# Kernel optimization log

Hardware: AMD Instinct MI355X
Metric: run time of the kernel (lower is better)

## Reference

```python
import jax, jax.numpy as jnp
import numpy as np

B, S, QD, VD, H = 32, 2048, 1024, 1024, 1024
NEG = -1e9


def setup_inputs() -> dict:
    key = jax.random.key(0)
    ks = jax.random.split(key, 7)
    query = jax.random.normal(ks[0], (B, QD), dtype=jnp.float32)
    value = jax.random.normal(ks[1], (B, S, VD), dtype=jnp.float32)
    mask = jax.random.randint(ks[2], (B, S), 0, 2).astype(bool)
    # params (Linear weights stored as [in, out] for einsum convenience)
    Wq = jax.random.normal(ks[3], (QD, H), dtype=jnp.float32) / np.sqrt(QD)
    bq = jax.random.normal(ks[4], (H,), dtype=jnp.float32) * 0.01
    Wv = jax.random.normal(ks[5], (VD, H), dtype=jnp.float32) / np.sqrt(VD)
    w = jax.random.normal(ks[6], (H,), dtype=jnp.float32) / np.sqrt(H)
    return {"query": query, "value": value, "mask": mask,
            "Wq": Wq, "bq": bq, "Wv": Wv, "w": w}


def reference(query, value, mask, Wq, bq, Wv, w):
    # q-projection: [B, H]
    hq = query @ Wq + bq
    # v-projection: [B, S, H]
    hv = jnp.einsum('bsv,vh->bsh', value, Wv)
    # additive attention energies: [B, S]
    logits = jnp.einsum('bsh,h->bs', jnp.tanh(hq[:, None, :] + hv), w)
    logits = jnp.where(mask, logits, NEG)
    return jax.nn.softmax(logits, axis=-1)
```

## Files before the change

kernel.cpp:

```cpp
#include <hip/hip_runtime.h>
#include <hip/hip_bf16.h>
#include <hip/hip_fp16.h>

typedef _Float16 f16;
typedef _Float16 f16x8 __attribute__((ext_vector_type(8)));
typedef float f32x16 __attribute__((ext_vector_type(16)));
typedef unsigned int u32;

#define BB 32
#define SS 2048
#define HH 1024
#define KK 1024

#define WS_BP 0
#define WS_HQ (2u*1024u*1024u)
#define WS_LP (WS_HQ + 131072u)

__device__ __forceinline__ float tanh_f(float x) {
    float e = __expf(2.0f * x);
    return 1.0f - 2.0f * __builtin_amdgcn_rcpf(e + 1.0f);
}

__device__ __forceinline__ void gload_lds16(const void* g, void* l) {
    __builtin_amdgcn_global_load_lds(
        (const __attribute__((address_space(1))) u32*)g,
        (__attribute__((address_space(3))) u32*)l, 16, 0, 0);
}

__global__ void pack_wv(const float* __restrict__ Wv, f16* __restrict__ BP) {
    int i = blockIdx.x * 256 + threadIdx.x;
    int k = i >> 10, n = i & 1023;
    float v = Wv[i];
    int ntb = n >> 8;
    int ntl = (n >> 5) & 7;
    int kit = k >> 5;
    int ksl = (k >> 4) & 1;
    int lane = ((k >> 3) & 1) * 32 + (n & 31);
    int j = k & 7;
    BP[((((ntb * 32 + kit) * 8 + ntl) * 2 + ksl) * 64 + lane) * 8 + j] = (f16)v;
}

__global__ void hq_kernel(const float* __restrict__ query, const float* __restrict__ Wq,
                          const float* __restrict__ bq, float* __restrict__ hq) {
    int b = blockIdx.y;
    int h = (blockIdx.x & 3) * 256 + threadIdx.x;
    int v0 = (blockIdx.x >> 2) * 256;
    float acc = 0.f;
#pragma unroll 8
    for (int v = 0; v < 256; ++v)
        acc += query[b * 1024 + v0 + v] * Wq[(v0 + v) * 1024 + h];
    if (v0 == 0) acc += bq[h];
    atomicAdd(&hq[b * 1024 + h], acc);
}

__launch_bounds__(512, 4)
__global__ void fused_main(const float* __restrict__ value, const f16* __restrict__ BP,
                           const float* __restrict__ hq, const float* __restrict__ wvec,
                           float* __restrict__ lpart) {
    extern __shared__ char smem[];

    int bid = blockIdx.x;
    int tile = (bid & 7) * 256 + (bid >> 3);
    int Mt = tile >> 2, ntb = tile & 3;
    int m0 = Mt << 7;
    int b = m0 >> 11, s0 = m0 & 2047;

    int tid = threadIdx.x;
    int w = tid >> 6, l = tid & 63;
    int wm = w >> 2, wn = w & 3;
    int l31 = l & 31, lg = l >> 5;

    int arow = tid >> 2;
    const float* aga = value + (size_t)(m0 + arow) * 1024 + (tid & 3) * 8;
    int aw_off = arow * 64 + ((((tid & 3) ^ ((arow >> 1) & 3))) << 4);

    const char* bg = (const char*)BP + (size_t)ntb * (32u * 16384u) + tid * 16;

    int a_base[2], a_sw[2];
#pragma unroll
    for (int mt = 0; mt < 2; ++mt) {
        int row = wm * 64 + mt * 32 + l31;
        a_base[mt] = row * 64;
        a_sw[mt] = ((row >> 1) & 3) << 4;
    }
    int b_base[2];
#pragma unroll
    for (int nt = 0; nt < 2; ++nt)
        b_base[nt] = (wn * 2 + nt) * 2048 + l * 16;

    const f32x16 fzero = {};
    f32x16 acc[2][2];
#pragma unroll
    for (int mt = 0; mt < 2; ++mt)
#pragma unroll
        for (int nt = 0; nt < 2; ++nt) acc[mt][nt] = fzero;

    {
        const float4* ap = (const float4*)aga;
        float4 fa0 = ap[0], fa1 = ap[1];
        gload_lds16(bg, smem + 16384 + tid * 16);
        gload_lds16(bg + 8192, smem + 16384 + 8192 + tid * 16);
        union { f16 h[8]; uint4 u; } pk;
        pk.h[0] = (f16)fa0.x; pk.h[1] = (f16)fa0.y; pk.h[2] = (f16)fa0.z; pk.h[3] = (f16)fa0.w;
        pk.h[4] = (f16)fa1.x; pk.h[5] = (f16)fa1.y; pk.h[6] = (f16)fa1.z; pk.h[7] = (f16)fa1.w;
        *(uint4*)(smem + aw_off) = pk.u;
        __syncthreads();
    }

#pragma unroll 1
    for (int t = 0; t < 32; ++t) {
        const char* Acur = smem + (t & 1) * 8192;
        const char* Bcur = smem + 16384 + (t & 1) * 16384;
        char* Anx = smem + ((t + 1) & 1) * 8192;
        char* Bnx = smem + 16384 + ((t + 1) & 1) * 16384;

        float4 fa0, fa1;
        if (t < 31) {
            const float4* ap = (const float4*)(aga + (t + 1) * 32);
            fa0 = ap[0]; fa1 = ap[1];
            const char* bsrc = bg + (size_t)(t + 1) * 16384;
            gload_lds16(bsrc, Bnx + tid * 16);
            gload_lds16(bsrc + 8192, Bnx + 8192 + tid * 16);
        }

#pragma unroll
        for (int ks = 0; ks < 2; ++ks) {
            int sl = (ks * 2 + lg) << 4;
            f16x8 av0 = *(const f16x8*)(Acur + a_base[0] + (sl ^ a_sw[0]));
            f16x8 av1 = *(const f16x8*)(Acur + a_base[1] + (sl ^ a_sw[1]));
            f16x8 bv0 = *(const f16x8*)(Bcur + b_base[0] + ks * 1024);
            f16x8 bv1 = *(const f16x8*)(Bcur + b_base[1] + ks * 1024);
            acc[0][0] = __builtin_amdgcn_mfma_f32_32x32x16_f16(av0, bv0, acc[0][0], 0, 0, 0);
            acc[0][1] = __builtin_amdgcn_mfma_f32_32x32x16_f16(av0, bv1, acc[0][1], 0, 0, 0);
            acc[1][0] = __builtin_amdgcn_mfma_f32_32x32x16_f16(av1, bv0, acc[1][0], 0, 0, 0);
            acc[1][1] = __builtin_amdgcn_mfma_f32_32x32x16_f16(av1, bv1, acc[1][1], 0, 0, 0);
        }

        if (t < 31) {
            union { f16 h[8]; uint4 u; } pk;
            pk.h[0] = (f16)fa0.x; pk.h[1] = (f16)fa0.y; pk.h[2] = (f16)fa0.z; pk.h[3] = (f16)fa0.w;
            pk.h[4] = (f16)fa1.x; pk.h[5] = (f16)fa1.y; pk.h[6] = (f16)fa1.z; pk.h[7] = (f16)fa1.w;
            *(uint4*)(Anx + aw_off) = pk.u;
        }
        __syncthreads();
    }

    int h0 = ntb * 256 + wn * 64 + l31;
    int h1 = h0 + 32;
    float hq0 = hq[b * 1024 + h0], hq1 = hq[b * 1024 + h1];
    float w0 = wvec[h0], w1 = wvec[h1];

    float* part = (float*)smem;
#pragma unroll
    for (int mt = 0; mt < 2; ++mt) {
#pragma unroll
        for (int r = 0; r < 16; ++r) {
            float p = tanh_f(hq0 + acc[mt][0][r]) * w0
                    + tanh_f(hq1 + acc[mt][1][r]) * w1;
            p += __shfl_xor(p, 1); p += __shfl_xor(p, 2); p += __shfl_xor(p, 4);
            p += __shfl_xor(p, 8); p += __shfl_xor(p, 16);
            if (l31 == 0) {
                int row = wm * 64 + mt * 32 + (r & 3) + ((r >> 2) << 3) + (lg << 2);
                part[wn * 128 + row] = p;
            }
        }
    }
    __syncthreads();
    if (tid < 128) {
        float s = part[tid] + part[128 + tid] + part[256 + tid] + part[384 + tid];
        lpart[((size_t)ntb * 32 + b) * 2048 + s0 + tid] = s;
    }
}

__global__ void softmax_kernel(const float* __restrict__ lp, const int* __restrict__ mask,
                               float* __restrict__ out) {
    __shared__ float redm[16];
    __shared__ float reds[16];
    const int P = 32 * 2048;
    int b = blockIdx.x, t = threadIdx.x;
    int wid = t >> 6, lane = t & 63;
    int i0 = b * 2048 + t, i1 = i0 + 1024;
    float l0 = lp[i0] + lp[P + i0] + lp[2 * P + i0] + lp[3 * P + i0];
    float l1 = lp[i1] + lp[P + i1] + lp[2 * P + i1] + lp[3 * P + i1];
    float a0 = mask[i0] ? l0 : -1e9f;
    float a1 = mask[i1] ? l1 : -1e9f;
    float mx = fmaxf(a0, a1);
#pragma unroll
    for (int off = 1; off < 64; off <<= 1) mx = fmaxf(mx, __shfl_xor(mx, off));
    if (lane == 0) redm[wid] = mx;
    __syncthreads();
    mx = redm[0];
#pragma unroll
    for (int i = 1; i < 16; ++i) mx = fmaxf(mx, redm[i]);
    float e0 = __expf(a0 - mx), e1 = __expf(a1 - mx);
    float s = e0 + e1;
#pragma unroll
    for (int off = 1; off < 64; off <<= 1) s += __shfl_xor(s, off);
    if (lane == 0) reds[wid] = s;
    __syncthreads();
    float tot = 0.f;
#pragma unroll
    for (int i = 0; i < 16; ++i) tot += reds[i];
    float inv = 1.0f / tot;
    out[b * 2048 + t] = e0 * inv;
    out[b * 2048 + 1024 + t] = e1 * inv;
}

extern "C" void kernel_launch(void* const* d_in, const int* in_sizes, int n_in,
                              void* d_out, int out_size, void* d_ws, size_t ws_size,
                              hipStream_t stream) {
    const float* query = (const float*)d_in[0];
    const float* value = (const float*)d_in[1];
    const int*   mask  = (const int*)d_in[2];
    const float* Wq    = (const float*)d_in[3];
    const float* bq    = (const float*)d_in[4];
    const float* Wv    = (const float*)d_in[5];
    const float* wv    = (const float*)d_in[6];

    char* ws = (char*)d_ws;
    f16*   BP    = (f16*)(ws + WS_BP);
    float* hq    = (float*)(ws + WS_HQ);
    float* lpart = (float*)(ws + WS_LP);
    float* out   = (float*)d_out;

    hipMemsetAsync(hq, 0, BB * HH * sizeof(float), stream);
    pack_wv<<<(KK * HH) / 256, 256, 0, stream>>>(Wv, BP);
    hq_kernel<<<dim3(16, BB), 256, 0, stream>>>(query, Wq, bq, hq);
    fused_main<<<2048, 512, 49152, stream>>>(value, BP, hq, wv, lpart);
    softmax_kernel<<<BB, 1024, 0, stream>>>(lpart, mask, out);
}
```

Baseline: 228.6 us.

## Deepen GEMM main loop pipelining with manual waitcnt, setprio, and paired epilogue shuffles

Unrolls the K loop by two with explicit ping-pong buffers, prefetches the A operand two steps ahead in registers, and replaces __syncthreads with fine-grained s_waitcnt vmcnt(2)/lgkmcnt(0) plus s_barrier so the next B tile's global-to-LDS loads can stay in flight across the barrier. Raises wave priority around the MFMA block and uses sched_barrier to pin instruction order. The epilogue reduces two rows per shuffle chain to halve the number of cross-lane reduction steps. The manual wait counts are fragile and the clamped tail indices issue redundant loads.

```diff
diff --git a/kernel.cpp b/kernel.cpp
--- a/kernel.cpp
+++ b/kernel.cpp
@@ -25,6 +25,13 @@
     __builtin_amdgcn_global_load_lds(
         (const __attribute__((address_space(1))) u32*)g,
         (__attribute__((address_space(3))) u32*)l, 16, 0, 0);
+}
+
+__device__ __forceinline__ void write_a16(char* dst, int off, float4 va, float4 vb) {
+    union { f16 h[8]; uint4 u; } pk;
+    pk.h[0] = (f16)va.x; pk.h[1] = (f16)va.y; pk.h[2] = (f16)va.z; pk.h[3] = (f16)va.w;
+    pk.h[4] = (f16)vb.x; pk.h[5] = (f16)vb.y; pk.h[6] = (f16)vb.z; pk.h[7] = (f16)vb.w;
+    *(uint4*)(dst + off) = pk.u;
 }
 
 __global__ void pack_wv(const float* __restrict__ Wv, f16* __restrict__ BP) {
@@ -58,6 +65,10 @@
                            const float* __restrict__ hq, const float* __restrict__ wvec,
                            float* __restrict__ lpart) {
     extern __shared__ char smem[];
+    char* A0 = smem;
+    char* A1 = smem + 8192;
+    char* B0 = smem + 16384;
+    char* B1 = smem + 32768;
 
     int bid = blockIdx.x;
     int tile = (bid & 7) * 256 + (bid >> 3);
@@ -95,54 +106,69 @@
 #pragma unroll
         for (int nt = 0; nt < 2; ++nt) acc[mt][nt] = fzero;
 
+#define COMPUTE(Acur, Bcur) do { \
+        __builtin_amdgcn_s_setprio(1); \
+        _Pragma("unroll") \
+        for (int ks = 0; ks < 2; ++ks) { \
+            int sl = (ks * 2 + lg) << 4; \
+            f16x8 av0 = *(const f16x8*)((Acur) + a_base[0] + (sl ^ a_sw[0])); \
+            f16x8 av1 = *(const f16x8*)((Acur) + a_base[1] + (sl ^ a_sw[1])); \
+            f16x8 bv0 = *(const f16x8*)((Bcur) + b_base[0] + ks * 1024); \
+            f16x8 bv1 = *(const f16x8*)((Bcur) + b_base[1] + ks * 1024); \
+            acc[0][0] = __builtin_amdgcn_mfma_f32_32x32x16_f16(av0, bv0, acc[0][0], 0, 0, 0); \
+            acc[0][1] = __builtin_amdgcn_mfma_f32_32x32x16_f16(av0, bv1, acc[0][1], 0, 0, 0); \
+            acc[1][0] = __builtin_amdgcn_mfma_f32_32x32x16_f16(av1, bv0, acc[1][0], 0, 0, 0); \
+            acc[1][1] = __builtin_amdgcn_mfma_f32_32x32x16_f16(av1, bv1, acc[1][1], 0, 0, 0); \
+        } \
+        __builtin_amdgcn_s_setprio(0); \
+    } while (0)
+
+    float4 fe0, fe1, fo0, fo1;
+
     {
+        gload_lds16(bg, B0 + tid * 16);
+        gload_lds16(bg + 8192, B0 + 8192 + tid * 16);
+        __builtin_amdgcn_sched_barrier(0);
         const float4* ap = (const float4*)aga;
-        float4 fa0 = ap[0], fa1 = ap[1];
-        gload_lds16(bg, smem + 16384 + tid * 16);
-        gload_lds16(bg + 8192, smem + 16384 + 8192 + tid * 16);
-        union { f16 h[8]; uint4 u; } pk;
-        pk.h[0] = (f16)fa0.x; pk.h[1] = (f16)fa0.y; pk.h[2] = (f16)fa0.z; pk.h[3] = (f16)fa0.w;
-        pk.h[4] = (f16)fa1.x; pk.h[5] = (f16)fa1.y; pk.h[6] = (f16)fa1.z; pk.h[7] = (f16)fa1.w;
-        *(uint4*)(smem + aw_off) = pk.u;
-        __syncthreads();
+        float4 e0 = ap[0], e1 = ap[1];
+        write_a16(A0, aw_off, e0, e1);
+        const float4* ap1 = (const float4*)(aga + 32);
+        fo0 = ap1[0]; fo1 = ap1[1];
+        asm volatile("s_waitcnt lgkmcnt(0)" ::: "memory");
+        __builtin_amdgcn_s_barrier();
     }
 
 #pragma unroll 1
-    for (int t = 0; t < 32; ++t) {
-        const char* Acur = smem + (t & 1) * 8192;
-        const char* Bcur = smem + 16384 + (t & 1) * 16384;
-        char* Anx = smem + ((t + 1) & 1) * 8192;
-        char* Bnx = smem + 16384 + ((t + 1) & 1) * 16384;
-
-        float4 fa0, fa1;
-        if (t < 31) {
-            const float4* ap = (const float4*)(aga + (t + 1) * 32);
-            fa0 = ap[0]; fa1 = ap[1];
-            const char* bsrc = bg + (size_t)(t + 1) * 16384;
-            gload_lds16(bsrc, Bnx + tid * 16);
-            gload_lds16(bsrc + 8192, Bnx + 8192 + tid * 16);
+    for (int tt = 0; tt < 16; ++tt) {
+        {
+            const char* bsrc = bg + (size_t)(2 * tt + 1) * 16384;
+            gload_lds16(bsrc, B1 + tid * 16);
+            gload_lds16(bsrc + 8192, B1 + 8192 + tid * 16);
+            __builtin_amdgcn_sched_barrier(0);
+            int xa = 2 * tt + 2; if (xa > 31) xa = 31;
+            const float4* ap = (const float4*)(aga + xa * 32);
+            fe0 = ap[0]; fe1 = ap[1];
+            __builtin_amdgcn_sched_barrier(0);
+            COMPUTE(A0, B0);
+            write_a16(A1, aw_off, fo0, fo1);
+            asm volatile("s_waitcnt vmcnt(2) lgkmcnt(0)" ::: "memory");
+            __builtin_amdgcn_s_barrier();
         }
-
-#pragma unroll
-        for (int ks = 0; ks < 2; ++ks) {
-            int sl = (ks * 2 + lg) << 4;
-            f16x8 av0 = *(const f16x8*)(Acur + a_base[0] + (sl ^ a_sw[0]));
-            f16x8 av1 = *(const f16x8*)(Acur + a_base[1] + (sl ^ a_sw[1]));
-            f16x8 bv0 = *(const f16x8*)(Bcur + b_base[0] + ks * 1024);
-            f16x8 bv1 = *(const f16x8*)(Bcur + b_base[1] + ks * 1024);
-            acc[0][0] = __builtin_amdgcn_mfma_f32_32x32x16_f16(av0, bv0, acc[0][0], 0, 0, 0);
-            acc[0][1] = __builtin_amdgcn_mfma_f32_32x32x16_f16(av0, bv1, acc[0][1], 0, 0, 0);
-            acc[1][0] = __builtin_amdgcn_mfma_f32_32x32x16_f16(av1, bv0, acc[1][0], 0, 0, 0);
-            acc[1][1] = __builtin_amdgcn_mfma_f32_32x32x16_f16(av1, bv1, acc[1][1], 0, 0, 0);
+        {
+            int xb = 2 * tt + 2; if (xb > 31) xb = 31;
+            const char* bsrc = bg + (size_t)xb * 16384;
+            gload_lds16(bsrc, B0 + tid * 16);
+            gload_lds16(bsrc + 8192, B0 + 8192 + tid * 16);
+            __builtin_amdgcn_sched_barrier(0);
+            int xc = 2 * tt + 3; if (xc > 31) xc = 31;
+            const float4* ap = (const float4*)(aga + xc * 32);
+            fo0 = ap[0]; fo1 = ap[1];
+            __builtin_amdgcn_sched_barrier(0);
+            COMPUTE(A1, B1);
+            if (tt < 15) write_a16(A0, aw_off, fe0, fe1);
+            asm volatile("s_waitcnt vmcnt(2) lgkmcnt(0)" ::: "memory");
+            __builtin_amdgcn_s_barrier();
         }
-
-        if (t < 31) {
-            union { f16 h[8]; uint4 u; } pk;
-            pk.h[0] = (f16)fa0.x; pk.h[1] = (f16)fa0.y; pk.h[2] = (f16)fa0.z; pk.h[3] = (f16)fa0.w;
-            pk.h[4] = (f16)fa1.x; pk.h[5] = (f16)fa1.y; pk.h[6] = (f16)fa1.z; pk.h[7] = (f16)fa1.w;
-            *(uint4*)(Anx + aw_off) = pk.u;
-        }
-        __syncthreads();
     }
 
     int h0 = ntb * 256 + wn * 64 + l31;
@@ -154,14 +180,19 @@
 #pragma unroll
     for (int mt = 0; mt < 2; ++mt) {
 #pragma unroll
-        for (int r = 0; r < 16; ++r) {
-            float p = tanh_f(hq0 + acc[mt][0][r]) * w0
-                    + tanh_f(hq1 + acc[mt][1][r]) * w1;
-            p += __shfl_xor(p, 1); p += __shfl_xor(p, 2); p += __shfl_xor(p, 4);
-            p += __shfl_xor(p, 8); p += __shfl_xor(p, 16);
-            if (l31 == 0) {
+        for (int i = 0; i < 8; ++i) {
+            float pa = tanh_f(hq0 + acc[mt][0][2 * i]) * w0
+                     + tanh_f(hq1 + acc[mt][1][2 * i]) * w1;
+            float pb = tanh_f(hq0 + acc[mt][0][2 * i + 1]) * w0
+                     + tanh_f(hq1 + acc[mt][1][2 * i + 1]) * w1;
+            float ea = __shfl_xor(pa, 1), eb = __shfl_xor(pb, 1);
+            float g = (l & 1) ? (pb + eb) : (pa + ea);
+            g += __shfl_xor(g, 2); g += __shfl_xor(g, 4);
+            g += __shfl_xor(g, 8); g += __shfl_xor(g, 16);
+            if (l31 < 2) {
+                int r = 2 * i + (l31 & 1);
                 int row = wm * 64 + mt * 32 + (r & 3) + ((r >> 2) << 3) + (lg << 2);
-                part[wn * 128 + row] = p;
+                part[wn * 128 + row] = g;
             }
         }
     }
@@ -170,6 +201,7 @@
         float s = part[tid] + part[128 + tid] + part[256 + tid] + part[384 + tid];
         lpart[((size_t)ntb * 32 + b) * 2048 + s0 + tid] = s;
     }
+#undef COMPUTE
 }
 
 __global__ void softmax_kernel(const float* __restrict__ lp, const int* __restrict__ mask,
@@ -223,7 +255,7 @@
     float* lpart = (float*)(ws + WS_LP);
     float* out   = (float*)d_out;
 
-    hipMemsetAsync(hq, 0, BB * HH * sizeof(float), stream);
+    (void)hipMemsetAsync(hq, 0, BB * HH * sizeof(float), stream);
     pack_wv<<<(KK * HH) / 256, 256, 0, stream>>>(Wv, BP);
     hq_kernel<<<dim3(16, BB), 256, 0, stream>>>(query, Wq, bq, hq);
     fused_main<<<2048, 512, 49152, stream>>>(value, BP, hq, wv, lpart);
```

Result: faster. 217.3 us (-4.9%).
